# Kernel optimization log

Measured on AMD Instinct MI355X. Metric: run time of the kernel, lower is better.

Reference implementation:

```python
import jax, jax.numpy as jnp
import numpy as np

THETA = 10000.0
D_K = 128
MAX_SEQ_LEN = 4096
BATCH, N_HEADS, SEQ_LEN = 4, 16, 4096


def build_ro_weights(theta, d_k, max_seq_len, dtype=jnp.float32):
    # Block-diagonal 2x2 rotation matrices, identical math to the torch loop.
    k = jnp.arange(d_k // 2, dtype=dtype)                      # [d_k/2]
    pos = jnp.arange(max_seq_len, dtype=dtype)                 # [S]
    inv_freq = theta ** (-2.0 * k / d_k)                       # [d_k/2]
    ang = pos[:, None] * inv_freq[None, :]                     # [S, d_k/2]
    cos, sin = jnp.cos(ang), jnp.sin(ang)
    ev = 2 * jnp.arange(d_k // 2)
    od = ev + 1
    R = jnp.zeros((max_seq_len, d_k, d_k), dtype=dtype)
    R = R.at[:, ev, ev].set(cos)
    R = R.at[:, ev, od].set(-sin)
    R = R.at[:, od, ev].set(sin)
    R = R.at[:, od, od].set(cos)
    return R


def setup_inputs() -> dict:
    key = jax.random.key(0)
    kx, = jax.random.split(key, 1)
    x = jax.random.normal(kx, (BATCH, N_HEADS, SEQ_LEN, D_K), dtype=jnp.float32)
    token_positions = jnp.arange(SEQ_LEN, dtype=jnp.int64 if jax.config.jax_enable_x64 else jnp.int32)
    ro_weights = build_ro_weights(THETA, D_K, MAX_SEQ_LEN)
    return {"x": x, "token_positions": token_positions, "ro_weights": ro_weights}


def reference(x, token_positions, ro_weights):
    # Gather per-position rotation matrices, then batched matvec:
    # out[..., s, i] = sum_j ro_weights[pos[s], i, j] * x[..., s, j]
    R = ro_weights[token_positions]                # [S, d_k, d_k]
    return jnp.einsum('...sj,sij->...si', x, R)
```

## Files before the change

### kernel.cpp

```cpp
#include <hip/hip_runtime.h>
#include <hip/hip_bf16.h>


#define ROPE_D    128
#define ROPE_S    4096
#define ROPE_BH   64
#define ROPE_RSTR (128*128)

__global__ __launch_bounds__(256) void
RotaryPositionalEmbedding_68332929679843_kernel(const float* __restrict__ x,
                                                const int* __restrict__ pos,
                                                const float* __restrict__ R,
                                                float* __restrict__ out) {
    __shared__ float cs[ROPE_D];

    const int s = blockIdx.x;
    const int t = threadIdx.x;

    const long long p = (long long)pos[s];
    const float* Rp = R + p * (long long)ROPE_RSTR;
    if (t < 64) {
        cs[t] = Rp[t * 258];
    } else if (t < 128) {
        const int k = t - 64;
        cs[t] = Rp[k * 258 + 128];
    }
    __syncthreads();

    for (int it = 0; it < 8; ++it) {
        const int f  = it * 256 + t;
        const int bh = f >> 5;
        const int c4 = f & 31;
        const size_t idx = ((size_t)bh * ROPE_S + s) * ROPE_D + (size_t)c4 * 4;

        const float4 v = *(const float4*)(x + idx);
        const int k = c4 * 2;
        const float c0 = cs[k],     s0 = cs[64 + k];
        const float c1 = cs[k + 1], s1 = cs[64 + k + 1];

        float4 o;
        o.x = c0 * v.x - s0 * v.y;
        o.y = s0 * v.x + c0 * v.y;
        o.z = c1 * v.z - s1 * v.w;
        o.w = s1 * v.z + c1 * v.w;
        *(float4*)(out + idx) = o;
    }
}

extern "C" void kernel_launch(void* const* d_in, const int* in_sizes, int n_in,
                              void* d_out, int out_size, void* d_ws, size_t ws_size,
                              hipStream_t stream) {
    const float* x   = (const float*)d_in[0];
    const int*   tp  = (const int*)d_in[1];
    const float* R   = (const float*)d_in[2];
    float*       out = (float*)d_out;

    dim3 grid(ROPE_S);
    dim3 block(256);
    RotaryPositionalEmbedding_68332929679843_kernel<<<grid, block, 0, stream>>>(x, tp, R, out);
}
```

Before: 431.6 us.

## Split cos/sin gather into separate kernel and stream x linearly

Moves the per-position rotation coefficient gather into a pre-pass kernel that writes a compact cos/sin table to workspace. The apply kernel then processes x in fully linear order with 4 float4 elements per thread, reading coefficients from the L2-resident table. This removes the per-block shared-memory gather, the barrier, and the strided per-head access pattern, at the cost of an extra launch and a small workspace round trip.

```diff
diff --git a/kernel.cpp b/kernel.cpp
--- a/kernel.cpp
+++ b/kernel.cpp
@@ -4,46 +4,52 @@
 
 #define ROPE_D    128
 #define ROPE_S    4096
-#define ROPE_BH   64
 #define ROPE_RSTR (128*128)
+#define ROPE_N4   (4*16*4096*32)
 
 __global__ __launch_bounds__(256) void
-RotaryPositionalEmbedding_68332929679843_kernel(const float* __restrict__ x,
-                                                const int* __restrict__ pos,
-                                                const float* __restrict__ R,
-                                                float* __restrict__ out) {
-    __shared__ float cs[ROPE_D];
-
-    const int s = blockIdx.x;
-    const int t = threadIdx.x;
-
+rope_gather_cs_kernel(const int* __restrict__ pos,
+                      const float* __restrict__ R,
+                      float* __restrict__ cs) {
+    const int i = blockIdx.x * 256 + threadIdx.x;
+    const int s = i >> 7;
+    const int j = i & 127;
     const long long p = (long long)pos[s];
     const float* Rp = R + p * (long long)ROPE_RSTR;
-    if (t < 64) {
-        cs[t] = Rp[t * 258];
-    } else if (t < 128) {
-        const int k = t - 64;
-        cs[t] = Rp[k * 258 + 128];
+    float v;
+    if (j < 64) {
+        v = Rp[j * 258];
+    } else {
+        const int k = j - 64;
+        v = Rp[k * 258 + 128];
     }
-    __syncthreads();
+    cs[i] = v;
+}
 
-    for (int it = 0; it < 8; ++it) {
-        const int f  = it * 256 + t;
-        const int bh = f >> 5;
-        const int c4 = f & 31;
-        const size_t idx = ((size_t)bh * ROPE_S + s) * ROPE_D + (size_t)c4 * 4;
+__global__ __launch_bounds__(256) void
+rope_apply_kernel(const float* __restrict__ x,
+                  const float* __restrict__ cs,
+                  float* __restrict__ out) {
+    const int base = blockIdx.x * 1024 + threadIdx.x;
+#pragma unroll
+    for (int it = 0; it < 4; ++it) {
+        const int i4 = base + it * 256;
+        const int row = i4 >> 5;
+        const int s   = row & (ROPE_S - 1);
+        const int c4  = i4 & 31;
+        const int k   = c4 * 2;
 
-        const float4 v = *(const float4*)(x + idx);
-        const int k = c4 * 2;
-        const float c0 = cs[k],     s0 = cs[64 + k];
-        const float c1 = cs[k + 1], s1 = cs[64 + k + 1];
+        const float4 v = *(const float4*)(x + (size_t)i4 * 4);
+        const float* csp = cs + s * ROPE_D;
+        const float c0 = csp[k],      s0 = csp[64 + k];
+        const float c1 = csp[k + 1],  s1 = csp[64 + k + 1];
 
         float4 o;
         o.x = c0 * v.x - s0 * v.y;
         o.y = s0 * v.x + c0 * v.y;
         o.z = c1 * v.z - s1 * v.w;
         o.w = s1 * v.z + c1 * v.w;
-        *(float4*)(out + idx) = o;
+        *(float4*)(out + (size_t)i4 * 4) = o;
     }
 }
 
@@ -54,8 +60,8 @@
     const int*   tp  = (const int*)d_in[1];
     const float* R   = (const float*)d_in[2];
     float*       out = (float*)d_out;
+    float*       cs  = (float*)d_ws;
 
-    dim3 grid(ROPE_S);
-    dim3 block(256);
-    RotaryPositionalEmbedding_68332929679843_kernel<<<grid, block, 0, stream>>>(x, tp, R, out);
+    rope_gather_cs_kernel<<<dim3(ROPE_S * ROPE_D / 256), dim3(256), 0, stream>>>(tp, R, cs);
+    rope_apply_kernel<<<dim3(ROPE_N4 / 1024), dim3(256), 0, stream>>>(x, cs, out);
 }
```

Result: faster. 420.6 us (-2.6%).
